# Kernel tuning notes

Measured on AMD Instinct MI355X. Metric: run time of the kernel, lower is better.

The kernel has to match this reference:

```python
import jax, jax.numpy as jnp
import numpy as np

D_INNER = 5120
DT_RANK = 160
N_STATE = 16
BATCH = 256


def _softplus_thresh20(x):
    # ttnn.softplus(parameter1=1.0, parameter2=20.0): linear above threshold 20
    return jnp.where(x > 20.0, x, jnp.log1p(jnp.exp(jnp.minimum(x, 20.0))))


def setup_inputs() -> dict:
    key = jax.random.key(0)
    ks = jax.random.split(key, 9)
    x = jax.random.normal(ks[0], (1, 1, BATCH, D_INNER), dtype=jnp.float32)
    # scale weights by 1/sqrt(fan_in) so softplus input is O(1)
    W_dt_low = jax.random.normal(ks[1], (D_INNER, DT_RANK), dtype=jnp.float32) / np.sqrt(D_INNER)
    W_dt = jax.random.normal(ks[2], (DT_RANK, D_INNER), dtype=jnp.float32) / np.sqrt(DT_RANK)
    b_dt = jax.random.normal(ks[3], (D_INNER,), dtype=jnp.float32)
    W_B = jax.random.normal(ks[4], (D_INNER, N_STATE), dtype=jnp.float32) / np.sqrt(D_INNER)
    W_C = jax.random.normal(ks[5], (D_INNER, N_STATE), dtype=jnp.float32) / np.sqrt(D_INNER)
    # A = -exp(A_log): strictly negative, as in the module's preprocess_A
    A = -jnp.exp(0.5 * jax.random.normal(ks[6], (D_INNER, N_STATE), dtype=jnp.float32))
    D = jax.random.normal(ks[7], (D_INNER,), dtype=jnp.float32)
    h0 = 0.1 * jax.random.normal(ks[8], (BATCH, D_INNER, N_STATE), dtype=jnp.float32)
    return {"x": x, "W_dt_low": W_dt_low, "W_dt": W_dt, "b_dt": b_dt,
            "W_B": W_B, "W_C": W_C, "A": A, "D": D, "h0": h0}


def reference(x, W_dt_low, W_dt, b_dt, W_B, W_C, A, D, h0):
    b, d = x.shape[2], x.shape[3]
    xb = x.reshape(b, d)                                  # (B, D)
    # delta = softplus(x @ x_proj_dt @ dt_proj + bias)
    delta = _softplus_thresh20(xb @ W_dt_low @ W_dt + b_dt)   # (B, D)
    Bp = xb @ W_B                                         # (B, N)
    Cp = xb @ W_C                                         # (B, N)
    # discretize: abar = exp(delta * A), bbar = delta * B
    # layout (B, D, N) matches repeat_interleave(delta, n) / repeat(B, d)
    abar = jnp.exp(delta[:, :, None] * A[None, :, :])     # (B, D, N)
    bbar = delta[:, :, None] * Bp[:, None, :]             # (B, D, N)
    h = abar * h0 + bbar * xb[:, :, None]                 # (B, D, N)
    y = jnp.einsum('bdn,bn->bd', h, Cp)                   # reduce over state
    out = xb * D[None, :] + y                             # (B, D)
    return out.reshape(1, 1, b, d)
```

## Files before the change

### kernel.cpp

```cpp
#include <hip/hip_runtime.h>
#include <math.h>

#define D_INNER 5120
#define DT_RANK 160
#define N_STATE 16
#define BATCH   256
#define KTOT    192

#define BGRP    8
#define NBG     (BATCH / BGRP)
#define DDBLK   160
#define NDDB    (D_INNER / DDBLK)
#define SPLIT   32

#define K3_BT   8

#define OFF_T     0
#define SZ_T      (BATCH * KTOT)
#define OFF_P     (OFF_T + SZ_T)
#define SZ_P      (SPLIT * BATCH * KTOT)

__global__ __launch_bounds__(256) void k1_gemm(const float* __restrict__ x,
                                               const float* __restrict__ Wdtlow,
                                               const float* __restrict__ WB,
                                               const float* __restrict__ WC,
                                               float* __restrict__ ws) {
    __shared__ float lds[4 * BGRP * KTOT];
    const int tid  = threadIdx.x;
    const int lane = tid & 63;
    const int wv   = tid >> 6;
    const int b0   = blockIdx.x * BGRP;
    const int ddB  = blockIdx.y * DDBLK;

    float* xs = lds;
    for (int j = tid; j < (BGRP * DDBLK) / 4; j += 256) {
        int i  = j / (DDBLK / 4);
        int c4 = j % (DDBLK / 4);
        float4 v = *(const float4*)(x + (size_t)(b0 + i) * D_INNER + ddB + c4 * 4);
        *(float4*)(xs + i * DDBLK + c4 * 4) = v;
    }
    __syncthreads();

    const int dd0 = wv * 40;
    const float* p0 = Wdtlow + (size_t)(ddB + dd0) * DT_RANK + lane;
    const float* p1 = p0 + 64;
    const float* p2;
    int st2;
    if (lane < 32)      { p2 = p0 + 128;                                          st2 = DT_RANK; }
    else if (lane < 48) { p2 = WB + (size_t)(ddB + dd0) * N_STATE + (lane - 32);  st2 = N_STATE; }
    else                { p2 = WC + (size_t)(ddB + dd0) * N_STATE + (lane - 48);  st2 = N_STATE; }

    float acc0[BGRP], acc1[BGRP], acc2[BGRP];
#pragma unroll
    for (int i = 0; i < BGRP; ++i) { acc0[i] = 0.f; acc1[i] = 0.f; acc2[i] = 0.f; }

#pragma unroll 2
    for (int g = 0; g < 10; ++g) {
        float w0[4], w1[4], w2[4];
#pragma unroll
        for (int u = 0; u < 4; ++u) {
            int dd = g * 4 + u;
            w0[u] = p0[(size_t)dd * DT_RANK];
            w1[u] = p1[(size_t)dd * DT_RANK];
            w2[u] = p2[(size_t)dd * st2];
        }
#pragma unroll
        for (int i = 0; i < BGRP; ++i) {
            float4 xv = *(const float4*)(xs + i * DDBLK + dd0 + g * 4);
            acc0[i] += xv.x * w0[0] + xv.y * w0[1] + xv.z * w0[2] + xv.w * w0[3];
            acc1[i] += xv.x * w1[0] + xv.y * w1[1] + xv.z * w1[2] + xv.w * w1[3];
            acc2[i] += xv.x * w2[0] + xv.y * w2[1] + xv.z * w2[2] + xv.w * w2[3];
        }
    }
    __syncthreads();

#pragma unroll
    for (int i = 0; i < BGRP; ++i) {
        float* r = lds + wv * (BGRP * KTOT) + i * KTOT;
        r[lane]       = acc0[i];
        r[lane + 64]  = acc1[i];
        r[lane + 128] = acc2[i];
    }
    __syncthreads();

    float* P = ws + OFF_P + (size_t)blockIdx.y * (BATCH * KTOT) + (size_t)b0 * KTOT;
#pragma unroll
    for (int r = 0; r < 6; ++r) {
        int idx = tid + r * 256;
        P[idx] = lds[idx] + lds[idx + 1536] + lds[idx + 3072] + lds[idx + 4608];
    }
}

__global__ __launch_bounds__(256) void k2_reduce(float* __restrict__ ws) {
    int g = blockIdx.x * 256 + threadIdx.x;
    const float* P = ws + OFF_P;
    float a = 0.f;
#pragma unroll
    for (int s = 0; s < SPLIT; ++s) a += P[(size_t)s * (BATCH * KTOT) + g];
    ws[OFF_T + g] = a;
}

__global__ __launch_bounds__(256) void k3_fused(const float* __restrict__ Wdt,
                                                const float* __restrict__ b_dt,
                                                const float* __restrict__ x,
                                                const float* __restrict__ A,
                                                const float* __restrict__ Dv,
                                                const float* __restrict__ h0,
                                                const float* __restrict__ ws,
                                                float* __restrict__ out) {
    __shared__ float ts[DT_RANK * K3_BT];
    const int tid = threadIdx.x;
    const int d   = blockIdx.x * 256 + tid;
    const int b0  = blockIdx.y * K3_BT;
    const float* T = ws + OFF_T;

    for (int j = tid; j < DT_RANK * K3_BT; j += 256) {
        int b = j & (K3_BT - 1);
        int k = j >> 3;
        ts[j] = T[(size_t)(b0 + b) * KTOT + k];
    }
    __syncthreads();

    float acc[K3_BT];
#pragma unroll
    for (int i = 0; i < K3_BT; ++i) acc[i] = 0.f;

#pragma unroll 4
    for (int k = 0; k < DT_RANK; ++k) {
        float w = Wdt[(size_t)k * D_INNER + d];
        float4 t0 = *(const float4*)(ts + k * 8);
        float4 t1 = *(const float4*)(ts + k * 8 + 4);
        acc[0] += t0.x * w; acc[1] += t0.y * w; acc[2] += t0.z * w; acc[3] += t0.w * w;
        acc[4] += t1.x * w; acc[5] += t1.y * w; acc[6] += t1.z * w; acc[7] += t1.w * w;
    }

    const float bv = b_dt[d];
    const float Dd = Dv[d];
    const float4* a4 = (const float4*)(A + (size_t)d * N_STATE);
    float4 a0 = a4[0], a1 = a4[1], a2 = a4[2], a3 = a4[3];

#pragma unroll
    for (int i = 0; i < K3_BT; ++i) {
        const int b = b0 + i;
        float v     = acc[i] + bv;
        float delta = (v > 20.f) ? v : log1pf(__expf(v));

        const float* Tb = T + (size_t)b * KTOT;
        float sbc = 0.f;
#pragma unroll
        for (int n = 0; n < N_STATE; ++n) sbc += Tb[160 + n] * Tb[176 + n];

        const float4* h4 = (const float4*)(h0 + ((size_t)b * D_INNER + d) * N_STATE);
        float4 h_0 = h4[0], h_1 = h4[1], h_2 = h4[2], h_3 = h4[3];

        float y = 0.f;
        y += __expf(delta * a0.x) * h_0.x * Tb[176 + 0];
        y += __expf(delta * a0.y) * h_0.y * Tb[176 + 1];
        y += __expf(delta * a0.z) * h_0.z * Tb[176 + 2];
        y += __expf(delta * a0.w) * h_0.w * Tb[176 + 3];
        y += __expf(delta * a1.x) * h_1.x * Tb[176 + 4];
        y += __expf(delta * a1.y) * h_1.y * Tb[176 + 5];
        y += __expf(delta * a1.z) * h_1.z * Tb[176 + 6];
        y += __expf(delta * a1.w) * h_1.w * Tb[176 + 7];
        y += __expf(delta * a2.x) * h_2.x * Tb[176 + 8];
        y += __expf(delta * a2.y) * h_2.y * Tb[176 + 9];
        y += __expf(delta * a2.z) * h_2.z * Tb[176 + 10];
        y += __expf(delta * a2.w) * h_2.w * Tb[176 + 11];
        y += __expf(delta * a3.x) * h_3.x * Tb[176 + 12];
        y += __expf(delta * a3.y) * h_3.y * Tb[176 + 13];
        y += __expf(delta * a3.z) * h_3.z * Tb[176 + 14];
        y += __expf(delta * a3.w) * h_3.w * Tb[176 + 15];

        float xv = x[(size_t)b * D_INNER + d];
        out[(size_t)b * D_INNER + d] = xv * (Dd + delta * sbc) + y;
    }
}

extern "C" void kernel_launch(void* const* d_in, const int* in_sizes, int n_in,
                              void* d_out, int out_size, void* d_ws, size_t ws_size,
                              hipStream_t stream) {
    const float* x      = (const float*)d_in[0];
    const float* Wdtlow = (const float*)d_in[1];
    const float* Wdt    = (const float*)d_in[2];
    const float* bdt    = (const float*)d_in[3];
    const float* WB     = (const float*)d_in[4];
    const float* WC     = (const float*)d_in[5];
    const float* A      = (const float*)d_in[6];
    const float* Dv     = (const float*)d_in[7];
    const float* h0     = (const float*)d_in[8];
    float* ws  = (float*)d_ws;
    float* out = (float*)d_out;

    hipLaunchKernelGGL(k1_gemm, dim3(NBG, NDDB), dim3(256), 0, stream,
                       x, Wdtlow, WB, WC, ws);
    hipLaunchKernelGGL(k2_reduce, dim3((BATCH * KTOT) / 256), dim3(256), 0, stream, ws);
    hipLaunchKernelGGL(k3_fused, dim3(D_INNER / 256, BATCH / K3_BT), dim3(256),
                       0, stream, Wdt, bdt, x, A, Dv, h0, ws, out);
}
```

Before: 183.1 us.

## Restructure fused kernel into single-wave blocks with 4-batch tiles and early h0 prefetch

The fused dt-projection and state-update kernel now uses 64-thread blocks, each covering 4 batch rows instead of 8. The LDS staging of the low-rank activations and the block barrier are removed; each lane reads T directly from global memory through wave-uniform addresses. The h0 state loads for all four batch rows are issued up front, before the output math, so the large h0 stream is in flight earlier. In exchange, the Wdt row reads are repeated across twice as many batch tiles, and there are more, smaller blocks.

After: 183.7 us. No clear change (+0.3%).

```diff
diff --git a/kernel.cpp b/kernel.cpp
--- a/kernel.cpp
+++ b/kernel.cpp
@@ -13,7 +13,7 @@
 #define NDDB    (D_INNER / DDBLK)
 #define SPLIT   32
 
-#define K3_BT   8
+#define K3_BT   4
 
 #define OFF_T     0
 #define SZ_T      (BATCH * KTOT)
@@ -100,76 +100,75 @@
     ws[OFF_T + g] = a;
 }
 
-__global__ __launch_bounds__(256) void k3_fused(const float* __restrict__ Wdt,
-                                                const float* __restrict__ b_dt,
-                                                const float* __restrict__ x,
-                                                const float* __restrict__ A,
-                                                const float* __restrict__ Dv,
-                                                const float* __restrict__ h0,
-                                                const float* __restrict__ ws,
-                                                float* __restrict__ out) {
-    __shared__ float ts[DT_RANK * K3_BT];
-    const int tid = threadIdx.x;
-    const int d   = blockIdx.x * 256 + tid;
-    const int b0  = blockIdx.y * K3_BT;
+__global__ __launch_bounds__(64, 4) void k3_fused(const float* __restrict__ Wdt,
+                                                  const float* __restrict__ b_dt,
+                                                  const float* __restrict__ x,
+                                                  const float* __restrict__ A,
+                                                  const float* __restrict__ Dv,
+                                                  const float* __restrict__ h0,
+                                                  const float* __restrict__ ws,
+                                                  float* __restrict__ out) {
+    const int lane = threadIdx.x;
+    const int d    = blockIdx.x * 64 + lane;
+    const int b0   = blockIdx.y * K3_BT;
     const float* T = ws + OFF_T;
 
-    for (int j = tid; j < DT_RANK * K3_BT; j += 256) {
-        int b = j & (K3_BT - 1);
-        int k = j >> 3;
-        ts[j] = T[(size_t)(b0 + b) * KTOT + k];
-    }
-    __syncthreads();
+    const float* t0 = T + (size_t)(b0 + 0) * KTOT;
+    const float* t1 = T + (size_t)(b0 + 1) * KTOT;
+    const float* t2 = T + (size_t)(b0 + 2) * KTOT;
+    const float* t3 = T + (size_t)(b0 + 3) * KTOT;
 
-    float acc[K3_BT];
-#pragma unroll
-    for (int i = 0; i < K3_BT; ++i) acc[i] = 0.f;
-
-#pragma unroll 4
+    float acc[K3_BT] = {0.f, 0.f, 0.f, 0.f};
+#pragma unroll 8
     for (int k = 0; k < DT_RANK; ++k) {
         float w = Wdt[(size_t)k * D_INNER + d];
-        float4 t0 = *(const float4*)(ts + k * 8);
-        float4 t1 = *(const float4*)(ts + k * 8 + 4);
-        acc[0] += t0.x * w; acc[1] += t0.y * w; acc[2] += t0.z * w; acc[3] += t0.w * w;
-        acc[4] += t1.x * w; acc[5] += t1.y * w; acc[6] += t1.z * w; acc[7] += t1.w * w;
+        acc[0] += t0[k] * w;
+        acc[1] += t1[k] * w;
+        acc[2] += t2[k] * w;
+        acc[3] += t3[k] * w;
     }
 
-    const float bv = b_dt[d];
-    const float Dd = Dv[d];
+    float4 h[K3_BT][4];
+#pragma unroll
+    for (int i = 0; i < K3_BT; ++i) {
+        const float4* h4 = (const float4*)(h0 + ((size_t)(b0 + i) * D_INNER + d) * N_STATE);
+        h[i][0] = h4[0]; h[i][1] = h4[1]; h[i][2] = h4[2]; h[i][3] = h4[3];
+    }
+
+    const float bdt = b_dt[d];
+    const float Dd  = Dv[d];
     const float4* a4 = (const float4*)(A + (size_t)d * N_STATE);
     float4 a0 = a4[0], a1 = a4[1], a2 = a4[2], a3 = a4[3];
 
 #pragma unroll
     for (int i = 0; i < K3_BT; ++i) {
         const int b = b0 + i;
-        float v     = acc[i] + bv;
+        const float* Tb = T + (size_t)b * KTOT;
+
+        float v     = acc[i] + bdt;
         float delta = (v > 20.f) ? v : log1pf(__expf(v));
 
-        const float* Tb = T + (size_t)b * KTOT;
         float sbc = 0.f;
 #pragma unroll
         for (int n = 0; n < N_STATE; ++n) sbc += Tb[160 + n] * Tb[176 + n];
 
-        const float4* h4 = (const float4*)(h0 + ((size_t)b * D_INNER + d) * N_STATE);
-        float4 h_0 = h4[0], h_1 = h4[1], h_2 = h4[2], h_3 = h4[3];
-
         float y = 0.f;
-        y += __expf(delta * a0.x) * h_0.x * Tb[176 + 0];
-        y += __expf(delta * a0.y) * h_0.y * Tb[176 + 1];
-        y += __expf(delta * a0.z) * h_0.z * Tb[176 + 2];
-        y += __expf(delta * a0.w) * h_0.w * Tb[176 + 3];
-        y += __expf(delta * a1.x) * h_1.x * Tb[176 + 4];
-        y += __expf(delta * a1.y) * h_1.y * Tb[176 + 5];
-        y += __expf(delta * a1.z) * h_1.z * Tb[176 + 6];
-        y += __expf(delta * a1.w) * h_1.w * Tb[176 + 7];
-        y += __expf(delta * a2.x) * h_2.x * Tb[176 + 8];
-        y += __expf(delta * a2.y) * h_2.y * Tb[176 + 9];
-        y += __expf(delta * a2.z) * h_2.z * Tb[176 + 10];
-        y += __expf(delta * a2.w) * h_2.w * Tb[176 + 11];
-        y += __expf(delta * a3.x) * h_3.x * Tb[176 + 12];
-        y += __expf(delta * a3.y) * h_3.y * Tb[176 + 13];
-        y += __expf(delta * a3.z) * h_3.z * Tb[176 + 14];
-        y += __expf(delta * a3.w) * h_3.w * Tb[176 + 15];
+        y += __expf(delta * a0.x) * h[i][0].x * Tb[176 + 0];
+        y += __expf(delta * a0.y) * h[i][0].y * Tb[176 + 1];
+        y += __expf(delta * a0.z) * h[i][0].z * Tb[176 + 2];
+        y += __expf(delta * a0.w) * h[i][0].w * Tb[176 + 3];
+        y += __expf(delta * a1.x) * h[i][1].x * Tb[176 + 4];
+        y += __expf(delta * a1.y) * h[i][1].y * Tb[176 + 5];
+        y += __expf(delta * a1.z) * h[i][1].z * Tb[176 + 6];
+        y += __expf(delta * a1.w) * h[i][1].w * Tb[176 + 7];
+        y += __expf(delta * a2.x) * h[i][2].x * Tb[176 + 8];
+        y += __expf(delta * a2.y) * h[i][2].y * Tb[176 + 9];
+        y += __expf(delta * a2.z) * h[i][2].z * Tb[176 + 10];
+        y += __expf(delta * a2.w) * h[i][2].w * Tb[176 + 11];
+        y += __expf(delta * a3.x) * h[i][3].x * Tb[176 + 12];
+        y += __expf(delta * a3.y) * h[i][3].y * Tb[176 + 13];
+        y += __expf(delta * a3.z) * h[i][3].z * Tb[176 + 14];
+        y += __expf(delta * a3.w) * h[i][3].w * Tb[176 + 15];
 
         float xv = x[(size_t)b * D_INNER + d];
         out[(size_t)b * D_INNER + d] = xv * (Dd + delta * sbc) + y;
@@ -194,6 +193,6 @@
     hipLaunchKernelGGL(k1_gemm, dim3(NBG, NDDB), dim3(256), 0, stream,
                        x, Wdtlow, WB, WC, ws);
     hipLaunchKernelGGL(k2_reduce, dim3((BATCH * KTOT) / 256), dim3(256), 0, stream, ws);
-    hipLaunchKernelGGL(k3_fused, dim3(D_INNER / 256, BATCH / K3_BT), dim3(256),
+    hipLaunchKernelGGL(k3_fused, dim3(D_INNER / 64, BATCH / K3_BT), dim3(64),
                        0, stream, Wdt, bdt, x, A, Dv, h0, ws, out);
 }
```
